# Kernel optimization log

Measured on AMD Instinct MI355X. Metric: run time of the kernel, lower is better.

## Reference

```python
import jax, jax.numpy as jnp
import numpy as np

H = 64; W = 64; P = 16; NPH = 4; NPW = 4; PH = 16; PW = 16; ZD = 32; HD = 1024; UD = 3; B = 256


def affine_grid(theta, Ho, Wo):
    # torch F.affine_grid, align_corners=False. theta [N,2,3] -> grid [N,Ho,Wo,2]
    xs = (2.0 * jnp.arange(Wo, dtype=theta.dtype) + 1.0) / Wo - 1.0
    ys = (2.0 * jnp.arange(Ho, dtype=theta.dtype) + 1.0) / Ho - 1.0
    X, Y = jnp.meshgrid(xs, ys)  # [Ho,Wo] each, x varies along last axis
    base = jnp.stack([X, Y, jnp.ones_like(X)], axis=-1)  # [Ho,Wo,3]
    return jnp.einsum('nij,hwj->nhwi', theta, base)


def grid_sample(img, grid):
    # torch F.grid_sample bilinear, padding_mode='zeros', align_corners=False
    # img [N,H,W], grid [N,Ho,Wo,2] in [-1,1]
    Hi, Wi = img.shape[1], img.shape[2]
    x = (grid[..., 0] + 1.0) * Wi / 2.0 - 0.5
    y = (grid[..., 1] + 1.0) * Hi / 2.0 - 0.5
    x0 = jnp.floor(x); y0 = jnp.floor(y)
    wx = x - x0; wy = y - y0

    def gather(ix, iy):
        valid = (ix >= 0) & (ix < Wi) & (iy >= 0) & (iy < Hi)
        ixc = jnp.clip(ix, 0, Wi - 1).astype(jnp.int32)
        iyc = jnp.clip(iy, 0, Hi - 1).astype(jnp.int32)
        v = jax.vmap(lambda im, yy, xx: im[yy, xx])(img, iyc, ixc)
        return jnp.where(valid, v, 0.0)

    return (gather(x0, y0) * (1 - wx) * (1 - wy)
            + gather(x0 + 1, y0) * wx * (1 - wy)
            + gather(x0, y0 + 1) * (1 - wx) * wy
            + gather(x0 + 1, y0 + 1) * wx * wy)


def rot_tr(u):
    # rotTrMatrix: u [N,3] (angle, tx, ty) -> [N,2,3]
    c = jnp.cos(u[:, 0]); s = jnp.sin(u[:, 0])
    R = jnp.stack([jnp.stack([c, -s], -1), jnp.stack([s, c], -1)], -2)  # [N,2,2]
    return jnp.concatenate([R, u[:, 1:3, None]], axis=2)


def anchor_theta():
    # anchor_move: identity rotation + per-part grid-cell-center translations
    tx = (np.arange(NPW) * (W / NPW) + W / NPW / 2) / W - 0.5
    ty = (np.arange(NPH) * (H / NPH) + H / NPH / 2) / H - 0.5
    th = np.tile(np.concatenate([np.eye(2), np.zeros((2, 1))], axis=1)[None], (P, 1, 1)).astype(np.float32)
    for k in range(P):
        th[k, 0, 2] = tx[k % NPW]
        th[k, 1, 2] = ty[k // NPW]
    return jnp.asarray(th)


def forward(inputs, W1, b1, W2, b2, Wum, bum, Wuv, buv, Wgm, bgm, Wgv, bgv, Wz, M, eps_u, eps_g):
    hid = jax.nn.relu(inputs.reshape(-1, H * W) @ W1 + b1)
    hid = jax.nn.relu(hid @ W2 + b2)
    # global transform distribution (note: F.threshold(x,-6,6) -> 6 where x<=-6)
    gmu = jnp.tanh(hid @ Wgm + bgm)
    gpre = hid @ Wgv + bgv
    gvar = jnp.exp(jnp.where(gpre > -6.0, gpre, 6.0))
    gu = gmu + gvar * eps_g  # sample_u uses mu + var*eps (var, not std) as in source
    # per-part transform distribution (F.threshold(x,-6,-6) -> clamp below at -6)
    umu = jnp.tanh(hid @ Wum + bum)
    upre = hid @ Wuv + buv
    uvar = jnp.exp(jnp.where(upre > -6.0, upre, -6.0))
    u = (umu + uvar * eps_u).reshape(-1, UD)  # [B*P,3]
    # decode parts (input is ones, as in source)
    parts = jax.nn.sigmoid(jnp.ones((B, ZD), inputs.dtype) @ Wz).reshape(B * P, PH, PW)
    padh = (H - PH) // 2; padw = (W - PW) // 2
    parts = jnp.pad(parts, ((0, 0), (padh, H - PH - padh), (padw, W - PW - padw)))
    # anchor placement of parts and kernel masks
    th_a = jnp.tile(anchor_theta(), (B, 1, 1))  # [B*P,2,3], part-minor ordering
    g_a = affine_grid(th_a, H, W)
    parts = grid_sample(parts, g_a)                     # [B*P,H,W]
    KM = grid_sample(M[:B * P].reshape(B * P, H, W), g_a)
    # per-part rotation+translation for parts; translation-only for kernel
    theta = rot_tr(u)                                   # [B*P,2,3]
    g = affine_grid(theta, H, W)
    eye = jnp.broadcast_to(jnp.eye(2, dtype=theta.dtype), (B * P, 2, 2))
    theta_K = jnp.concatenate([eye, theta[:, :, 2:3]], axis=2)
    g_K = affine_grid(theta_K, H, W)
    KM = grid_sample(KM, g_K).reshape(B, P, H, W)
    xp = grid_sample(parts, g).reshape(B, P, H, W)
    # masked weighted compositing
    num = jnp.sum(xp * KM, axis=1)
    den = jnp.sum(KM, axis=1)
    den = jnp.where(den == 0.0, 1.0, den)
    x = num / den
    # global transform
    theta_g = rot_tr(gu)
    g_g = affine_grid(theta_g, H, W)
    return grid_sample(x, g_g)[:, None]  # [B,1,H,W]


def setup_inputs() -> dict:
    key = jax.random.key(0)
    ks = jax.random.split(key, 18)

    def lin(k, fin, fout):
        return jax.random.normal(k, (fin, fout), jnp.float32) / np.sqrt(fin)

    return {
        'inputs': jax.random.uniform(ks[0], (B, H * W), jnp.float32),
        'W1': lin(ks[1], H * W, HD), 'b1': jnp.zeros((HD,), jnp.float32),
        'W2': lin(ks[2], HD, HD), 'b2': jnp.zeros((HD,), jnp.float32),
        'Wum': lin(ks[3], HD, P * UD), 'bum': jnp.zeros((P * UD,), jnp.float32),
        'Wuv': lin(ks[4], HD, P * UD), 'buv': jnp.zeros((P * UD,), jnp.float32),
        'Wgm': lin(ks[5], HD, UD), 'bgm': jnp.zeros((UD,), jnp.float32),
        'Wgv': lin(ks[6], HD, UD), 'bgv': jnp.zeros((UD,), jnp.float32),
        'Wz': lin(ks[7], ZD, P * PH * PW),
        'M': jax.random.uniform(ks[8], (B * P, 1, H, W), jnp.float32),
        'eps_u': jax.random.normal(ks[9], (B, P * UD), jnp.float32),
        'eps_g': jax.random.normal(ks[10], (B, UD), jnp.float32),
    }


def reference(inputs, W1, b1, W2, b2, Wum, bum, Wuv, buv, Wgm, bgm, Wgv, bgv, Wz, M, eps_u, eps_g):
    return forward(inputs, W1, b1, W2, b2, Wum, bum, Wuv, buv, Wgm, bgm, Wgv, bgv, Wz, M, eps_u, eps_g)
```

## Files before the change

kernel.cpp:

```cpp
#include <hip/hip_runtime.h>
#include <math.h>

#define SPLITK 8

typedef __bf16 bf16x8 __attribute__((ext_vector_type(8)));
typedef float  f32x4  __attribute__((ext_vector_type(4)));

__device__ inline unsigned short bf16rne(float x) {
    unsigned int u = __float_as_uint(x);
    unsigned int r = u + 0x7FFFu + ((u >> 16) & 1u);
    return (unsigned short)(r >> 16);
}
__device__ inline float bf16tof(unsigned short h) {
    return __uint_as_float(((unsigned int)h) << 16);
}

__global__ __launch_bounds__(256) void prep_all(
    const float* __restrict__ inputs,
    const float* __restrict__ W1, const float* __restrict__ W2,
    const float* __restrict__ Wum, const float* __restrict__ Wuv,
    const float* __restrict__ Wgm, const float* __restrict__ Wgv,
    const float* __restrict__ Wz,
    unsigned short* __restrict__ Ahi, unsigned short* __restrict__ Alo,
    unsigned short* __restrict__ W1Thi, unsigned short* __restrict__ W1Tlo,
    unsigned short* __restrict__ W2Thi, unsigned short* __restrict__ W2Tlo,
    float* __restrict__ WT, float* __restrict__ partsb)
{
    __shared__ float t[32][33];
    int bid = blockIdx.x;
    int tid = threadIdx.x;
    if (bid < 4096 || (bid >= 8192 && bid < 9216)) {
        const float* W = (bid < 4096) ? W1 : W2;
        unsigned short* Thi = (bid < 4096) ? W1Thi : W2Thi;
        unsigned short* Tlo = (bid < 4096) ? W1Tlo : W2Tlo;
        int K = (bid < 4096) ? 4096 : 1024;
        int b2 = (bid < 4096) ? bid : (bid - 8192);
        int n0 = (b2 & 31) * 32, k0 = (b2 >> 5) * 32;
        int c = tid & 31, r0 = tid >> 5;
#pragma unroll
        for (int i = 0; i < 4; i++)
            t[r0 + 8 * i][c] = W[(size_t)(k0 + r0 + 8 * i) * 1024 + n0 + c];
        __syncthreads();
        int kk = tid & 31, n1 = tid >> 5;
#pragma unroll
        for (int i = 0; i < 4; i++) {
            float x = t[kk][n1 + 8 * i];
            unsigned short h = bf16rne(x);
            unsigned short l = bf16rne(x - bf16tof(h));
            size_t o = (size_t)(n0 + n1 + 8 * i) * K + k0 + kk;
            Thi[o] = h;
            Tlo[o] = l;
        }
    } else if (bid < 8192) {
        int id = (bid - 4096) * 256 + tid;
        float x = inputs[id];
        unsigned short h = bf16rne(x);
        Ahi[id] = h;
        Alo[id] = bf16rne(x - bf16tof(h));
    } else if (bid < 9624) {
        int id = (bid - 9216) * 256 + tid;
        int o = id >> 10;
        int k = id & 1023;
        float v;
        if (o < 48)       v = Wum[k * 48 + o];
        else if (o < 96)  v = Wuv[k * 48 + (o - 48)];
        else if (o < 99)  v = Wgm[k * 3 + (o - 96)];
        else              v = Wgv[k * 3 + (o - 99)];
        WT[id] = v;
    } else {
        int idx = (bid - 9624) * 256 + tid;
        float s = 0.f;
#pragma unroll
        for (int z = 0; z < 32; z++) s += Wz[z * 4096 + idx];
        partsb[idx] = 1.f / (1.f + expf(-s));
    }
}

__global__ __launch_bounds__(256) void gemm_bf16x3(
    const unsigned short* __restrict__ Ahi, const unsigned short* __restrict__ Alo,
    const unsigned short* __restrict__ Bhi, const unsigned short* __restrict__ Blo,
    float* __restrict__ psum, int K, int kchunk)
{
    __shared__ unsigned short Ah[4096], Al[4096], Bh[4096], Bl[4096];
    int tid = threadIdx.x;
    int n0 = blockIdx.x * 64, m0 = blockIdx.y * 64;
    int kb = blockIdx.z * kchunk;
    int wid = tid >> 6, lane = tid & 63;
    int wm = wid & 1, wn = wid >> 1;
    int lm = lane & 15, q = lane >> 4;

    int r0 = tid >> 3, ch0 = tid & 7;
    int r1 = (tid + 256) >> 3, ch1 = (tid + 256) & 7;
    int l0 = r0 * 64 + 8 * (ch0 ^ (r0 & 7));
    int l1 = r1 * 64 + 8 * (ch1 ^ (r1 & 7));
    size_t ga0 = (size_t)(m0 + r0) * K + kb + ch0 * 8;
    size_t ga1 = (size_t)(m0 + r1) * K + kb + ch1 * 8;
    size_t gb0 = (size_t)(n0 + r0) * K + kb + ch0 * 8;
    size_t gb1 = (size_t)(n0 + r1) * K + kb + ch1 * 8;

    f32x4 acc[2][2] = {};

    int nkt = kchunk >> 6;
    uint4 vah0, vah1, val0, val1, vbh0, vbh1, vbl0, vbl1;
    vah0 = *(const uint4*)(Ahi + ga0);
    vah1 = *(const uint4*)(Ahi + ga1);
    val0 = *(const uint4*)(Alo + ga0);
    val1 = *(const uint4*)(Alo + ga1);
    vbh0 = *(const uint4*)(Bhi + gb0);
    vbh1 = *(const uint4*)(Bhi + gb1);
    vbl0 = *(const uint4*)(Blo + gb0);
    vbl1 = *(const uint4*)(Blo + gb1);

    int frm0 = (wm * 32 + lm) * 64;
    int frm1 = (wm * 32 + 16 + lm) * 64;
    int frn0 = (wn * 32 + lm) * 64;
    int frn1 = (wn * 32 + 16 + lm) * 64;
    int sw = lm & 7;

    for (int kt = 0; kt < nkt; kt++) {
        __syncthreads();
        *(uint4*)(Ah + l0) = vah0;
        *(uint4*)(Ah + l1) = vah1;
        *(uint4*)(Al + l0) = val0;
        *(uint4*)(Al + l1) = val1;
        *(uint4*)(Bh + l0) = vbh0;
        *(uint4*)(Bh + l1) = vbh1;
        *(uint4*)(Bl + l0) = vbl0;
        *(uint4*)(Bl + l1) = vbl1;
        __syncthreads();
        if (kt + 1 < nkt) {
            size_t o = (size_t)(kt + 1) * 64;
            vah0 = *(const uint4*)(Ahi + ga0 + o);
            vah1 = *(const uint4*)(Ahi + ga1 + o);
            val0 = *(const uint4*)(Alo + ga0 + o);
            val1 = *(const uint4*)(Alo + ga1 + o);
            vbh0 = *(const uint4*)(Bhi + gb0 + o);
            vbh1 = *(const uint4*)(Bhi + gb1 + o);
            vbl0 = *(const uint4*)(Blo + gb0 + o);
            vbl1 = *(const uint4*)(Blo + gb1 + o);
        }
#pragma unroll
        for (int ks = 0; ks < 2; ks++) {
            int cidx = 8 * (((ks << 2) + q) ^ sw);
            bf16x8 ah0 = *(const bf16x8*)(Ah + frm0 + cidx);
            bf16x8 ah1 = *(const bf16x8*)(Ah + frm1 + cidx);
            bf16x8 al0 = *(const bf16x8*)(Al + frm0 + cidx);
            bf16x8 al1 = *(const bf16x8*)(Al + frm1 + cidx);
            bf16x8 bh0 = *(const bf16x8*)(Bh + frn0 + cidx);
            bf16x8 bh1 = *(const bf16x8*)(Bh + frn1 + cidx);
            bf16x8 bl0 = *(const bf16x8*)(Bl + frn0 + cidx);
            bf16x8 bl1 = *(const bf16x8*)(Bl + frn1 + cidx);
            acc[0][0] = __builtin_amdgcn_mfma_f32_16x16x32_bf16(ah0, bh0, acc[0][0], 0, 0, 0);
            acc[0][0] = __builtin_amdgcn_mfma_f32_16x16x32_bf16(ah0, bl0, acc[0][0], 0, 0, 0);
            acc[0][0] = __builtin_amdgcn_mfma_f32_16x16x32_bf16(al0, bh0, acc[0][0], 0, 0, 0);
            acc[0][1] = __builtin_amdgcn_mfma_f32_16x16x32_bf16(ah0, bh1, acc[0][1], 0, 0, 0);
            acc[0][1] = __builtin_amdgcn_mfma_f32_16x16x32_bf16(ah0, bl1, acc[0][1], 0, 0, 0);
            acc[0][1] = __builtin_amdgcn_mfma_f32_16x16x32_bf16(al0, bh1, acc[0][1], 0, 0, 0);
            acc[1][0] = __builtin_amdgcn_mfma_f32_16x16x32_bf16(ah1, bh0, acc[1][0], 0, 0, 0);
            acc[1][0] = __builtin_amdgcn_mfma_f32_16x16x32_bf16(ah1, bl0, acc[1][0], 0, 0, 0);
            acc[1][0] = __builtin_amdgcn_mfma_f32_16x16x32_bf16(al1, bh0, acc[1][0], 0, 0, 0);
            acc[1][1] = __builtin_amdgcn_mfma_f32_16x16x32_bf16(ah1, bh1, acc[1][1], 0, 0, 0);
            acc[1][1] = __builtin_amdgcn_mfma_f32_16x16x32_bf16(ah1, bl1, acc[1][1], 0, 0, 0);
            acc[1][1] = __builtin_amdgcn_mfma_f32_16x16x32_bf16(al1, bh1, acc[1][1], 0, 0, 0);
        }
    }

    float* op = psum + (size_t)blockIdx.z * (256 * 1024);
#pragma unroll
    for (int mt = 0; mt < 2; mt++)
#pragma unroll
        for (int nt = 0; nt < 2; nt++) {
            int row = m0 + wm * 32 + mt * 16 + q * 4;
            int col = n0 + wn * 32 + nt * 16 + lm;
#pragma unroll
            for (int r = 0; r < 4; r++)
                op[(size_t)(row + r) * 1024 + col] = acc[mt][nt][r];
        }
}

__global__ __launch_bounds__(256) void reduce_bias_relu(
    const float* __restrict__ psum, const float* __restrict__ bias,
    float* __restrict__ out)
{
    int i = blockIdx.x * 256 + threadIdx.x;
    float v = 0.f;
#pragma unroll
    for (int s = 0; s < SPLITK; s++) v += psum[(size_t)s * 262144 + i];
    v += bias[i & 1023];
    out[i] = fmaxf(v, 0.f);
}

__global__ __launch_bounds__(256) void reduce_bias_relu_split(
    const float* __restrict__ psum, const float* __restrict__ bias,
    unsigned short* __restrict__ hi, unsigned short* __restrict__ lo)
{
    int i = blockIdx.x * 256 + threadIdx.x;
    float v = 0.f;
#pragma unroll
    for (int s = 0; s < SPLITK; s++) v += psum[(size_t)s * 262144 + i];
    v += bias[i & 1023];
    v = fmaxf(v, 0.f);
    unsigned short h = bf16rne(v);
    hi[i] = h;
    lo[i] = bf16rne(v - bf16tof(h));
}

__global__ __launch_bounds__(512) void heads_v2(
    const float* __restrict__ hid, const float* __restrict__ WT,
    const float* __restrict__ bum, const float* __restrict__ buv,
    const float* __restrict__ bgm, const float* __restrict__ bgv,
    const float* __restrict__ eps_u, const float* __restrict__ eps_g,
    float* __restrict__ u_out, float* __restrict__ gu_out)
{
    int b = blockIdx.x;
    int tid = threadIdx.x;
    int w = tid >> 6, l = tid & 63;

    const float* hp = hid + b * 1024 + l * 4;
    float4 hr[4];
#pragma unroll
    for (int i = 0; i < 4; i++) hr[i] = *(const float4*)(hp + i * 256);

    int o = w;
    int rm = (o < 48) ? o : (48 + o);
    int rv = (o < 48) ? (o + 48) : (51 + o);
    float4 wm[4], wv[4];
    {
        const float* wp = WT + rm * 1024 + l * 4;
#pragma unroll
        for (int i = 0; i < 4; i++) wm[i] = *(const float4*)(wp + i * 256);
        wp = WT + rv * 1024 + l * 4;
#pragma unroll
        for (int i = 0; i < 4; i++) wv[i] = *(const float4*)(wp + i * 256);
    }

    while (o < 51) {
        int onext = o + 8;
        float4 wmn[4], wvn[4];
        if (onext < 51) {
            int rm2 = (onext < 48) ? onext : (48 + onext);
            int rv2 = (onext < 48) ? (onext + 48) : (51 + onext);
            const float* wp = WT + rm2 * 1024 + l * 4;
#pragma unroll
            for (int i = 0; i < 4; i++) wmn[i] = *(const float4*)(wp + i * 256);
            wp = WT + rv2 * 1024 + l * 4;
#pragma unroll
            for (int i = 0; i < 4; i++) wvn[i] = *(const float4*)(wp + i * 256);
        }
        float am = 0.f, av = 0.f;
#pragma unroll
        for (int i = 0; i < 4; i++) {
            am = fmaf(hr[i].x, wm[i].x, am);
            am = fmaf(hr[i].y, wm[i].y, am);
            am = fmaf(hr[i].z, wm[i].z, am);
            am = fmaf(hr[i].w, wm[i].w, am);
            av = fmaf(hr[i].x, wv[i].x, av);
            av = fmaf(hr[i].y, wv[i].y, av);
            av = fmaf(hr[i].z, wv[i].z, av);
            av = fmaf(hr[i].w, wv[i].w, av);
        }
#pragma unroll
        for (int s = 32; s; s >>= 1) {
            am += __shfl_xor(am, s, 64);
            av += __shfl_xor(av, s, 64);
        }
        if (l == 0) {
            if (o < 48) {
                float umu = tanhf(am + bum[o]);
                float uvar = expf(fmaxf(av + buv[o], -6.f));
                u_out[b * 48 + o] = umu + uvar * eps_u[b * 48 + o];
            } else {
                int n = o - 48;
                float gmu = tanhf(am + bgm[n]);
                float gpre = av + bgv[n];
                float gvar = expf(gpre > -6.f ? gpre : 6.f);
                gu_out[b * 3 + n] = gmu + gvar * eps_g[b * 3 + n];
            }
        }
#pragma unroll
        for (int i = 0; i < 4; i++) { wm[i] = wmn[i]; wv[i] = wvn[i]; }
        o = onext;
    }
}

__global__ __launch_bounds__(256) void composite_v6(
    const float* __restrict__ M, const float* __restrict__ parts,
    const float* __restrict__ u, float* __restrict__ xout)
{
    __shared__ float patch[4096];
    __shared__ float plane[2][17 * 64];
    __shared__ float pc[16], psn[16], ptx[16], pty[16];
    int b = blockIdx.x >> 2;
    int quarter = blockIdx.x & 3;
    int tid = threadIdx.x;
    int brow0 = quarter * 16;

    for (int i = tid; i < 4096; i += 256) patch[i] = parts[i];
    if (tid < 16) {
        const float* up = u + (b * 16 + tid) * 3;
        float ang = up[0];
        pc[tid] = cosf(ang);
        psn[tid] = sinf(ang);
        ptx[tid] = up[1];
        pty[tid] = up[2];
    }
    __syncthreads();

    int j = tid & 63;
    int i0 = brow0 + (tid >> 6) * 4;
    float xnv = (float)(2 * j + 1) * (1.f / 64.f) - 1.f;

    float num[4] = {}, den[4] = {};
    const float* Mb = M + ((size_t)(b * 16) << 12);

    auto calc_iy = [&](int p, int& iy, int& iY, float& wy) {
        int dy = 8 * (p >> 2) - 12;
        float ay = fminf(fmaxf(32.f * pty[p], -16384.f), 16384.f);
        float fay = floorf(ay);
        wy = ay - fay;
        iy = (int)fay;
        iY = iy + dy;
    };

    int rr0 = tid >> 4, c0 = tid & 15;
    int rr1 = (tid + 256) >> 4, c1 = (tid + 256) & 15;

    int iy_arr[17], iY_arr[17]; float wy_arr[17];
#pragma unroll
    for (int p = 0; p < 16; p++) calc_iy(p, iy_arr[p], iY_arr[p], wy_arr[p]);

    float4 pfA0, pfA1;
    {
        int lo = brow0 + iY_arr[0];
        pfA0 = *(const float4*)(Mb + (min(max(lo + rr0, 0), 63) << 6) + c0 * 4);
        if (tid < 16)
            pfA1 = *(const float4*)(Mb + (min(max(lo + rr1, 0), 63) << 6) + c1 * 4);
        float4* dst = (float4*)plane[0];
        dst[tid] = pfA0;
        if (tid < 16) dst[tid + 256] = pfA1;
    }
    {
        int lo = brow0 + iY_arr[1];
        const float* Mp = Mb + (1 << 12);
        pfA0 = *(const float4*)(Mp + (min(max(lo + rr0, 0), 63) << 6) + c0 * 4);
        if (tid < 16)
            pfA1 = *(const float4*)(Mp + (min(max(lo + rr1, 0), 63) << 6) + c1 * 4);
    }
    __syncthreads();

    for (int p = 0; p < 16; p++) {
        int cur = p & 1;
        if (p + 1 < 16) {
            float4* dst = (float4*)plane[1 - cur];
            dst[tid] = pfA0;
            if (tid < 16) dst[tid + 256] = pfA1;
        }
        if (p + 2 < 16) {
            int lo = brow0 + iY_arr[p + 2];
            const float* Mp = Mb + ((size_t)(p + 2) << 12);
            pfA0 = *(const float4*)(Mp + (min(max(lo + rr0, 0), 63) << 6) + c0 * 4);
            if (tid < 16)
                pfA1 = *(const float4*)(Mp + (min(max(lo + rr1, 0), 63) << 6) + c1 * 4);
        }

        int iy = iy_arr[p], iY = iY_arr[p];
        float wy = wy_arr[p];
        int dx = 8 * (p & 3) - 12;
        float c = pc[p], s = psn[p], tx = ptx[p];

        float ax = fminf(fmaxf(32.f * tx, -16384.f), 16384.f);
        float fax = floorf(ax);
        float wx = ax - fax;
        int ix = (int)fax;

        int x0 = j + ix;
        int X = x0 + dx;
        bool vc0 = ((unsigned)x0 < 64u) && ((unsigned)X < 64u);
        bool vc1 = ((unsigned)(x0 + 1) < 64u) && ((unsigned)(X + 1) < 64u);
        float w0 = vc0 ? (1.f - wx) : 0.f;
        float w1 = vc1 ? wx : 0.f;
        int Xc0 = min(max(X, 0), 63);
        int Xc1 = min(max(X + 1, 0), 63);

        const float* pl = plane[cur];
        float R[5];
#pragma unroll
        for (int r = 0; r < 5; r++) {
            int i = i0 + r;
            int y0i = i + iy;
            int ri = i + iY;
            bool vr = ((unsigned)y0i < 64u) && ((unsigned)ri < 64u);
            int lrow = (tid >> 6) * 4 + r;
            const float* row = pl + (lrow << 6);
            float val = fmaf(w0, row[Xc0], w1 * row[Xc1]);
            R[r] = vr ? val : 0.f;
        }

        float Ax = fmaf(c, xnv, tx);
        float Ay = fmaf(s, xnv, pty[p]);
        int ox = 24 - dx, oy = 24 - (8 * (p >> 2) - 12);
        const float* pp = patch + (p << 8);
#pragma unroll
        for (int r = 0; r < 4; r++) {
            int i = i0 + r;
            float km = fmaf(wy, R[r + 1] - R[r], R[r]);
            den[r] += km;

            float ynv = (float)(2 * i + 1) * (1.f / 64.f) - 1.f;
            float gx = fmaf(-s, ynv, Ax);
            float gy = fmaf(c, ynv, Ay);
            gx = fminf(fmaxf(gx, -8.f), 8.f);
            gy = fminf(fmaxf(gy, -8.f), 8.f);
            float xs = fmaf(gx, 32.f, 31.5f);
            float ysv = fmaf(gy, 32.f, 31.5f);
            float xf = floorf(xs), yf = floorf(ysv);
            float wxx = xs - xf, wyy = ysv - yf;
            int a0 = (int)yf - oy;
            int b0c = (int)xf - ox;
            if ((unsigned)(a0 + 1) <= 16u && (unsigned)(b0c + 1) <= 16u) {
                float v00 = 0.f, v10 = 0.f, v01 = 0.f, v11 = 0.f;
                if ((unsigned)a0 < 16u) {
                    const float* pr = pp + a0 * 16;
                    if ((unsigned)b0c < 16u) v00 = pr[b0c];
                    if ((unsigned)(b0c + 1) < 16u) v10 = pr[b0c + 1];
                }
                if ((unsigned)(a0 + 1) < 16u) {
                    const float* pr = pp + (a0 + 1) * 16;
                    if ((unsigned)b0c < 16u) v01 = pr[b0c];
                    if ((unsigned)(b0c + 1) < 16u) v11 = pr[b0c + 1];
                }
                float top = fmaf(wxx, v10 - v00, v00);
                float bot = fmaf(wxx, v11 - v01, v01);
                float xp = fmaf(wyy, bot - top, top);
                num[r] = fmaf(xp, km, num[r]);
            }
        }
        __syncthreads();
    }

    float* xo = xout + ((size_t)b << 12);
#pragma unroll
    for (int r = 0; r < 4; r++) {
        float d = (den[r] == 0.f) ? 1.f : den[r];
        xo[(i0 + r) * 64 + j] = num[r] / d;
    }
}

__global__ __launch_bounds__(256) void final_kernel(
    const float* __restrict__ xin, const float* __restrict__ gu,
    float* __restrict__ out)
{
    int id = blockIdx.x * 256 + threadIdx.x;
    int b = id >> 12;
    int pix = id & 4095;
    int ii = pix >> 6, jj = pix & 63;
    float ang = gu[b * 3 + 0], tx = gu[b * 3 + 1], ty = gu[b * 3 + 2];
    float c = cosf(ang), s = sinf(ang);
    float xn = (float)(2 * jj + 1) * (1.f / 64.f) - 1.f;
    float yn = (float)(2 * ii + 1) * (1.f / 64.f) - 1.f;
    float gx = c * xn - s * yn + tx;
    float gy = s * xn + c * yn + ty;
    float xs = (gx + 1.f) * 32.f - 0.5f;
    float ysv = (gy + 1.f) * 32.f - 0.5f;
    float xf = floorf(xs), yf = floorf(ysv);
    float wx = xs - xf, wy = ysv - yf;
    int x0 = (int)xf, y0 = (int)yf;
    const float* xp = xin + ((size_t)b << 12);
    float v00 = 0.f, v10 = 0.f, v01 = 0.f, v11 = 0.f;
    bool vx0 = (unsigned)x0 < 64u, vx1 = (unsigned)(x0 + 1) < 64u;
    if ((unsigned)y0 < 64u) {
        if (vx0) v00 = xp[y0 * 64 + x0];
        if (vx1) v10 = xp[y0 * 64 + x0 + 1];
    }
    if ((unsigned)(y0 + 1) < 64u) {
        if (vx0) v01 = xp[(y0 + 1) * 64 + x0];
        if (vx1) v11 = xp[(y0 + 1) * 64 + x0 + 1];
    }
    out[id] = v00 * (1.f - wx) * (1.f - wy) + v10 * wx * (1.f - wy)
            + v01 * (1.f - wx) * wy + v11 * wx * wy;
}

extern "C" void kernel_launch(void* const* d_in, const int* in_sizes, int n_in,
                              void* d_out, int out_size, void* d_ws, size_t ws_size,
                              hipStream_t stream)
{
    (void)in_sizes; (void)n_in; (void)out_size; (void)ws_size;
    const float* inputs = (const float*)d_in[0];
    const float* W1  = (const float*)d_in[1];
    const float* b1  = (const float*)d_in[2];
    const float* W2  = (const float*)d_in[3];
    const float* b2  = (const float*)d_in[4];
    const float* Wum = (const float*)d_in[5];
    const float* bum = (const float*)d_in[6];
    const float* Wuv = (const float*)d_in[7];
    const float* buv = (const float*)d_in[8];
    const float* Wgm = (const float*)d_in[9];
    const float* bgm = (const float*)d_in[10];
    const float* Wgv = (const float*)d_in[11];
    const float* bgv = (const float*)d_in[12];
    const float* Wz  = (const float*)d_in[13];
    const float* Mm  = (const float*)d_in[14];
    const float* eps_u = (const float*)d_in[15];
    const float* eps_g = (const float*)d_in[16];

    float* ws = (float*)d_ws;
    float* psum      = ws;
    float* hid2      = ws + 2097152;
    float* x_buf     = ws + 2359296;
    float* u_buf     = ws + 3407872;
    float* gu_buf    = ws + 3420160;
    float* parts_buf = ws + 3420928;
    float* WTh_buf   = ws + 3425024;
    unsigned short* us = (unsigned short*)(ws + 3529472);
    unsigned short* Ahi   = us;
    unsigned short* Alo   = Ahi + 1048576;
    unsigned short* W1Thi = Alo + 1048576;
    unsigned short* W1Tlo = W1Thi + 4194304;
    unsigned short* W2Thi = W1Tlo + 4194304;
    unsigned short* W2Tlo = W2Thi + 1048576;
    unsigned short* H1hi  = W2Tlo + 1048576;
    unsigned short* H1lo  = H1hi + 262144;

    prep_all<<<9640, 256, 0, stream>>>(inputs, W1, W2, Wum, Wuv, Wgm, Wgv, Wz,
                                       Ahi, Alo, W1Thi, W1Tlo, W2Thi, W2Tlo,
                                       WTh_buf, parts_buf);

    gemm_bf16x3<<<dim3(16, 4, SPLITK), 256, 0, stream>>>(Ahi, Alo, W1Thi, W1Tlo,
                                                         psum, 4096, 4096 / SPLITK);
    reduce_bias_relu_split<<<1024, 256, 0, stream>>>(psum, b1, H1hi, H1lo);
    gemm_bf16x3<<<dim3(16, 4, SPLITK), 256, 0, stream>>>(H1hi, H1lo, W2Thi, W2Tlo,
                                                         psum, 1024, 1024 / SPLITK);
    reduce_bias_relu<<<1024, 256, 0, stream>>>(psum, b2, hid2);
    heads_v2<<<256, 512, 0, stream>>>(hid2, WTh_buf, bum, buv, bgm, bgv,
                                      eps_u, eps_g, u_buf, gu_buf);
    composite_v6<<<1024, 256, 0, stream>>>(Mm, parts_buf, u_buf, x_buf);
    final_kernel<<<4096, 256, 0, stream>>>(x_buf, gu_buf, (float*)d_out);
}
```

Measured before the change: 210.2 us.

## Raise split-K for first GEMM and read mask rows directly in composite

The first GEMM's split-K factor goes from 8 to 16 while the second stays at 8. The reduce kernels now take the split count as a runtime argument, and the workspace offsets are moved to fit the larger partial-sum buffer. The composite kernel drops its double-buffered LDS staging of mask planes and the per-part __syncthreads, and reads mask rows straight from global memory. This trades LDS traffic and barriers for uncoalesced, cache-dependent gathers, and doubles the partial-sum writes and reads for the first GEMM.

```diff
diff --git a/kernel.cpp b/kernel.cpp
--- a/kernel.cpp
+++ b/kernel.cpp
@@ -1,7 +1,8 @@
 #include <hip/hip_runtime.h>
 #include <math.h>
 
-#define SPLITK 8
+#define SPLITK1 16
+#define SPLITK2 8
 
 typedef __bf16 bf16x8 __attribute__((ext_vector_type(8)));
 typedef float  f32x4  __attribute__((ext_vector_type(4)));
@@ -180,24 +181,22 @@
 
 __global__ __launch_bounds__(256) void reduce_bias_relu(
     const float* __restrict__ psum, const float* __restrict__ bias,
-    float* __restrict__ out)
+    float* __restrict__ out, int S)
 {
     int i = blockIdx.x * 256 + threadIdx.x;
     float v = 0.f;
-#pragma unroll
-    for (int s = 0; s < SPLITK; s++) v += psum[(size_t)s * 262144 + i];
+    for (int s = 0; s < S; s++) v += psum[(size_t)s * 262144 + i];
     v += bias[i & 1023];
     out[i] = fmaxf(v, 0.f);
 }
 
 __global__ __launch_bounds__(256) void reduce_bias_relu_split(
     const float* __restrict__ psum, const float* __restrict__ bias,
-    unsigned short* __restrict__ hi, unsigned short* __restrict__ lo)
+    unsigned short* __restrict__ hi, unsigned short* __restrict__ lo, int S)
 {
     int i = blockIdx.x * 256 + threadIdx.x;
     float v = 0.f;
-#pragma unroll
-    for (int s = 0; s < SPLITK; s++) v += psum[(size_t)s * 262144 + i];
+    for (int s = 0; s < S; s++) v += psum[(size_t)s * 262144 + i];
     v += bias[i & 1023];
     v = fmaxf(v, 0.f);
     unsigned short h = bf16rne(v);
@@ -283,17 +282,15 @@
     }
 }
 
-__global__ __launch_bounds__(256) void composite_v6(
+__global__ __launch_bounds__(256) void composite_v7(
     const float* __restrict__ M, const float* __restrict__ parts,
     const float* __restrict__ u, float* __restrict__ xout)
 {
     __shared__ float patch[4096];
-    __shared__ float plane[2][17 * 64];
     __shared__ float pc[16], psn[16], ptx[16], pty[16];
     int b = blockIdx.x >> 2;
     int quarter = blockIdx.x & 3;
     int tid = threadIdx.x;
-    int brow0 = quarter * 16;
 
     for (int i = tid; i < 4096; i += 256) patch[i] = parts[i];
     if (tid < 16) {
@@ -307,71 +304,27 @@
     __syncthreads();
 
     int j = tid & 63;
-    int i0 = brow0 + (tid >> 6) * 4;
+    int i0 = quarter * 16 + (tid >> 6) * 4;
     float xnv = (float)(2 * j + 1) * (1.f / 64.f) - 1.f;
 
     float num[4] = {}, den[4] = {};
     const float* Mb = M + ((size_t)(b * 16) << 12);
 
-    auto calc_iy = [&](int p, int& iy, int& iY, float& wy) {
+#pragma unroll 4
+    for (int p = 0; p < 16; p++) {
+        int dx = 8 * (p & 3) - 12;
         int dy = 8 * (p >> 2) - 12;
-        float ay = fminf(fmaxf(32.f * pty[p], -16384.f), 16384.f);
-        float fay = floorf(ay);
-        wy = ay - fay;
-        iy = (int)fay;
-        iY = iy + dy;
-    };
-
-    int rr0 = tid >> 4, c0 = tid & 15;
-    int rr1 = (tid + 256) >> 4, c1 = (tid + 256) & 15;
-
-    int iy_arr[17], iY_arr[17]; float wy_arr[17];
-#pragma unroll
-    for (int p = 0; p < 16; p++) calc_iy(p, iy_arr[p], iY_arr[p], wy_arr[p]);
-
-    float4 pfA0, pfA1;
-    {
-        int lo = brow0 + iY_arr[0];
-        pfA0 = *(const float4*)(Mb + (min(max(lo + rr0, 0), 63) << 6) + c0 * 4);
-        if (tid < 16)
-            pfA1 = *(const float4*)(Mb + (min(max(lo + rr1, 0), 63) << 6) + c1 * 4);
-        float4* dst = (float4*)plane[0];
-        dst[tid] = pfA0;
-        if (tid < 16) dst[tid + 256] = pfA1;
-    }
-    {
-        int lo = brow0 + iY_arr[1];
-        const float* Mp = Mb + (1 << 12);
-        pfA0 = *(const float4*)(Mp + (min(max(lo + rr0, 0), 63) << 6) + c0 * 4);
-        if (tid < 16)
-            pfA1 = *(const float4*)(Mp + (min(max(lo + rr1, 0), 63) << 6) + c1 * 4);
-    }
-    __syncthreads();
-
-    for (int p = 0; p < 16; p++) {
-        int cur = p & 1;
-        if (p + 1 < 16) {
-            float4* dst = (float4*)plane[1 - cur];
-            dst[tid] = pfA0;
-            if (tid < 16) dst[tid + 256] = pfA1;
-        }
-        if (p + 2 < 16) {
-            int lo = brow0 + iY_arr[p + 2];
-            const float* Mp = Mb + ((size_t)(p + 2) << 12);
-            pfA0 = *(const float4*)(Mp + (min(max(lo + rr0, 0), 63) << 6) + c0 * 4);
-            if (tid < 16)
-                pfA1 = *(const float4*)(Mp + (min(max(lo + rr1, 0), 63) << 6) + c1 * 4);
-        }
-
-        int iy = iy_arr[p], iY = iY_arr[p];
-        float wy = wy_arr[p];
-        int dx = 8 * (p & 3) - 12;
-        float c = pc[p], s = psn[p], tx = ptx[p];
+        float c = pc[p], s = psn[p], tx = ptx[p], ty = pty[p];
 
         float ax = fminf(fmaxf(32.f * tx, -16384.f), 16384.f);
         float fax = floorf(ax);
         float wx = ax - fax;
         int ix = (int)fax;
+        float ay = fminf(fmaxf(32.f * ty, -16384.f), 16384.f);
+        float fay = floorf(ay);
+        float wy = ay - fay;
+        int iy = (int)fay;
+        int iY = iy + dy;
 
         int x0 = j + ix;
         int X = x0 + dx;
@@ -382,23 +335,28 @@
         int Xc0 = min(max(X, 0), 63);
         int Xc1 = min(max(X + 1, 0), 63);
 
-        const float* pl = plane[cur];
+        const float* Mp = Mb + ((size_t)p << 12);
+        float v0[5], v1[5];
+#pragma unroll
+        for (int r = 0; r < 5; r++) {
+            int ri = i0 + r + iY;
+            int ric = min(max(ri, 0), 63);
+            const float* row = Mp + (ric << 6);
+            v0[r] = row[Xc0];
+            v1[r] = row[Xc1];
+        }
         float R[5];
 #pragma unroll
         for (int r = 0; r < 5; r++) {
             int i = i0 + r;
-            int y0i = i + iy;
-            int ri = i + iY;
-            bool vr = ((unsigned)y0i < 64u) && ((unsigned)ri < 64u);
-            int lrow = (tid >> 6) * 4 + r;
-            const float* row = pl + (lrow << 6);
-            float val = fmaf(w0, row[Xc0], w1 * row[Xc1]);
+            bool vr = ((unsigned)(i + iy) < 64u) && ((unsigned)(i + iY) < 64u);
+            float val = fmaf(w0, v0[r], w1 * v1[r]);
             R[r] = vr ? val : 0.f;
         }
 
         float Ax = fmaf(c, xnv, tx);
-        float Ay = fmaf(s, xnv, pty[p]);
-        int ox = 24 - dx, oy = 24 - (8 * (p >> 2) - 12);
+        float Ay = fmaf(s, xnv, ty);
+        int ox = 24 - dx, oy = 24 - dy;
         const float* pp = patch + (p << 8);
 #pragma unroll
         for (int r = 0; r < 4; r++) {
@@ -435,7 +393,6 @@
                 num[r] = fmaf(xp, km, num[r]);
             }
         }
-        __syncthreads();
     }
 
     float* xo = xout + ((size_t)b << 12);
@@ -505,13 +462,13 @@
 
     float* ws = (float*)d_ws;
     float* psum      = ws;
-    float* hid2      = ws + 2097152;
-    float* x_buf     = ws + 2359296;
-    float* u_buf     = ws + 3407872;
-    float* gu_buf    = ws + 3420160;
-    float* parts_buf = ws + 3420928;
-    float* WTh_buf   = ws + 3425024;
-    unsigned short* us = (unsigned short*)(ws + 3529472);
+    float* hid2      = ws + 4194304;
+    float* x_buf     = ws + 4456448;
+    float* u_buf     = ws + 5505024;
+    float* gu_buf    = ws + 5517312;
+    float* parts_buf = ws + 5518080;
+    float* WTh_buf   = ws + 5522176;
+    unsigned short* us = (unsigned short*)(ws + 5626624);
     unsigned short* Ahi   = us;
     unsigned short* Alo   = Ahi + 1048576;
     unsigned short* W1Thi = Alo + 1048576;
@@ -525,14 +482,14 @@
                                        Ahi, Alo, W1Thi, W1Tlo, W2Thi, W2Tlo,
                                        WTh_buf, parts_buf);
 
-    gemm_bf16x3<<<dim3(16, 4, SPLITK), 256, 0, stream>>>(Ahi, Alo, W1Thi, W1Tlo,
-                                                         psum, 4096, 4096 / SPLITK);
-    reduce_bias_relu_split<<<1024, 256, 0, stream>>>(psum, b1, H1hi, H1lo);
-    gemm_bf16x3<<<dim3(16, 4, SPLITK), 256, 0, stream>>>(H1hi, H1lo, W2Thi, W2Tlo,
-                                                         psum, 1024, 1024 / SPLITK);
-    reduce_bias_relu<<<1024, 256, 0, stream>>>(psum, b2, hid2);
+    gemm_bf16x3<<<dim3(16, 4, SPLITK1), 256, 0, stream>>>(Ahi, Alo, W1Thi, W1Tlo,
+                                                          psum, 4096, 4096 / SPLITK1);
+    reduce_bias_relu_split<<<1024, 256, 0, stream>>>(psum, b1, H1hi, H1lo, SPLITK1);
+    gemm_bf16x3<<<dim3(16, 4, SPLITK2), 256, 0, stream>>>(H1hi, H1lo, W2Thi, W2Tlo,
+                                                          psum, 1024, 1024 / SPLITK2);
+    reduce_bias_relu<<<1024, 256, 0, stream>>>(psum, b2, hid2, SPLITK2);
     heads_v2<<<256, 512, 0, stream>>>(hid2, WTh_buf, bum, buv, bgm, bgv,
                                       eps_u, eps_g, u_buf, gu_buf);
-    composite_v6<<<1024, 256, 0, stream>>>(Mm, parts_buf, u_buf, x_buf);
+    composite_v7<<<1024, 256, 0, stream>>>(Mm, parts_buf, u_buf, x_buf);
     final_kernel<<<4096, 256, 0, stream>>>(x_buf, gu_buf, (float*)d_out);
 }
```

Result: slower. 218.1 us (+3.8%).
